# Kernel tuning notes

Measured on AMD Instinct MI355X. Metric: run time of the kernel, lower is better.

Reference implementation:

```python
import jax, jax.numpy as jnp
import numpy as np

B, N, C, H = 8, 1024, 768, 12
D = C // H
SCALE = D ** -0.5


def setup_inputs() -> dict:
    key = jax.random.key(0)
    k1, k2, k3 = jax.random.split(key, 3)
    x = jax.random.normal(k1, (B, N, C), dtype=jnp.float32)
    w_qkv = jax.random.normal(k2, (C, 3 * C), dtype=jnp.float32) * (C ** -0.5)
    w_proj = jax.random.normal(k3, (C, C), dtype=jnp.float32) * (C ** -0.5)
    b_proj = jnp.zeros((C,), dtype=jnp.float32)
    return {"x": x, "w_qkv": w_qkv, "w_proj": w_proj, "b_proj": b_proj}


def reference(x, w_qkv, w_proj, b_proj):
    Bx, Nx, Cx = x.shape
    # qkv projection (no bias), split into q,k,v with shape [B, H, N, D]
    qkv = (x @ w_qkv).reshape(Bx, Nx, 3, H, D).transpose(2, 0, 3, 1, 4)
    q, k, v = qkv[0], qkv[1], qkv[2]
    # full attention matrix [B, H, N, N] (matches torch module's explicit materialization)
    attn = jnp.einsum('bhqd,bhkd->bhqk', q, k) * SCALE
    attn = jax.nn.softmax(attn, axis=-1)
    out = jnp.einsum('bhqk,bhkd->bhqd', attn, v)
    out = out.transpose(0, 2, 1, 3).reshape(Bx, Nx, Cx)
    return out @ w_proj + b_proj
```

## Files before the change

kernel.cpp:

```cpp
#include <hip/hip_runtime.h>


typedef unsigned short u16;
typedef short s16x8 __attribute__((ext_vector_type(8)));
typedef float f32x4 __attribute__((ext_vector_type(4)));
typedef u16   u16x8 __attribute__((ext_vector_type(8)));
typedef u16   u16x4 __attribute__((ext_vector_type(4)));

__device__ __forceinline__ u16 f2bf(float f) {
    unsigned int u = __builtin_bit_cast(unsigned int, f);
    u += 0x7FFFu + ((u >> 16) & 1u);
    return (u16)(u >> 16);
}

__device__ __forceinline__ void gload16(const u16* g, u16* l) {
    __builtin_amdgcn_global_load_lds(
        (const __attribute__((address_space(1))) unsigned int*)g,
        (__attribute__((address_space(3))) unsigned int*)l, 16, 0, 0);
}

__global__ __launch_bounds__(256) void prep(
    const float* __restrict__ x, u16* __restrict__ xb,
    const float* __restrict__ wq, u16* __restrict__ wqT,
    const float* __restrict__ wp, u16* __restrict__ wpT) {
    __shared__ float ts[32][33];
    const int g = blockIdx.x, tid = threadIdx.x;
    if (g < 3072) {
        const size_t i = ((size_t)g * 256 + tid) * 8;
        float4 v0 = *(const float4*)(x + i);
        float4 v1 = *(const float4*)(x + i + 4);
        u16x8 p;
        p[0] = f2bf(v0.x); p[1] = f2bf(v0.y); p[2] = f2bf(v0.z); p[3] = f2bf(v0.w);
        p[4] = f2bf(v1.x); p[5] = f2bf(v1.y); p[6] = f2bf(v1.z); p[7] = f2bf(v1.w);
        *(u16x8*)(xb + i) = p;
        return;
    }
    const float* in; u16* out; int K, Nc, n0, k0;
    if (g < 4800) {
        int gg = g - 3072; in = wq; out = wqT; K = 768; Nc = 2304;
        n0 = (gg % 72) * 32; k0 = (gg / 72) * 32;
    } else {
        int gg = g - 4800; in = wp; out = wpT; K = 768; Nc = 768;
        n0 = (gg % 24) * 32; k0 = (gg / 24) * 32;
    }
    const int tx = tid & 31, ty = tid >> 5;
#pragma unroll
    for (int j = 0; j < 4; ++j) {
        int r = ty + j * 8;
        ts[r][tx] = in[(size_t)(k0 + r) * Nc + n0 + tx];
    }
    __syncthreads();
#pragma unroll
    for (int j = 0; j < 4; ++j) {
        int r = ty + j * 8;
        out[(size_t)(n0 + r) * K + k0 + tx] = f2bf(ts[tx][r]);
    }
}

template<bool SWAP>
__device__ __forceinline__ void gemm_loop_128(
    f32x4 (&acc)[4][4], const u16* __restrict__ A, const u16* __restrict__ B,
    u16* As, u16* Bs, int m0, int n0, int lane, int w) {
    const int m15 = lane & 15, quad = lane >> 4;
    const int wy = w >> 1, wx = w & 1;
    const int qsw8 = (quad ^ ((m15 >> 1) & 3)) * 8;
    const int srow16 = lane >> 2;
    const int scg = ((lane & 3) ^ ((lane >> 3) & 3)) * 8;
    const size_t gA = (size_t)(m0 + w * 32 + srow16) * 768 + scg;
    const size_t gB = (size_t)(n0 + w * 32 + srow16) * 768 + scg;

    auto stage = [&](int buf, int s) {
        const int k0 = (s < 24 ? s : 0) * 32;
        u16* da = As + buf * 4096 + (w * 32) * 32;
        u16* db = Bs + buf * 4096 + (w * 32) * 32;
        gload16(A + gA + k0,            da);
        gload16(A + gA + 16 * 768 + k0, da + 16 * 32);
        gload16(B + gB + k0,            db);
        gload16(B + gB + 16 * 768 + k0, db + 16 * 32);
    };

    stage(0, 0);
    stage(1, 1);
    const int arow = (wy * 64 + m15) * 32 + qsw8;
    const int brow = (wx * 64 + m15) * 32 + qsw8;

#pragma unroll 3
    for (int s = 0; s < 24; ++s) {
        const int cur = s % 3;
        stage((s + 2) % 3, s + 2);
        asm volatile("s_waitcnt vmcnt(8)" ::: "memory");
        __builtin_amdgcn_s_barrier();
        const u16* Ap = As + cur * 4096;
        const u16* Bp = Bs + cur * 4096;
        s16x8 av[4], bv[4];
#pragma unroll
        for (int ri = 0; ri < 4; ++ri)
            av[ri] = *(const s16x8*)(Ap + arow + ri * 512);
#pragma unroll
        for (int ci = 0; ci < 4; ++ci)
            bv[ci] = *(const s16x8*)(Bp + brow + ci * 512);
        __builtin_amdgcn_s_setprio(1);
#pragma unroll
        for (int ri = 0; ri < 4; ++ri)
#pragma unroll
            for (int ci = 0; ci < 4; ++ci) {
                if (SWAP)
                    acc[ri][ci] = __builtin_amdgcn_mfma_f32_16x16x32_bf16(bv[ci], av[ri], acc[ri][ci], 0, 0, 0);
                else
                    acc[ri][ci] = __builtin_amdgcn_mfma_f32_16x16x32_bf16(av[ri], bv[ci], acc[ri][ci], 0, 0, 0);
            }
        __builtin_amdgcn_s_setprio(0);
        __builtin_amdgcn_s_barrier();
    }
    asm volatile("s_waitcnt vmcnt(0)" ::: "memory");
}

__global__ __launch_bounds__(256, 3) void gemm_qkv(
    const u16* __restrict__ Aq, const u16* __restrict__ Bt,
    u16* __restrict__ qb, u16* __restrict__ kb, u16* __restrict__ vbT) {
    __shared__ __align__(16) u16 As[3 * 128 * 32];
    __shared__ __align__(16) u16 Bs[3 * 128 * 32];
    const int tid = threadIdx.x;
    const int lane = tid & 63, w = tid >> 6;
    const int m15 = lane & 15, quad = lane >> 4;
    const int wy = w >> 1, wx = w & 1;
    const int g = blockIdx.x;
    const int xcd = g & 7, s = g >> 3;
    const int yt = xcd * 8 + (s & 7), xt = s >> 3;
    const int m0 = yt * 128, n0 = xt * 128;
    const int which = xt / 6;

    f32x4 acc[4][4] = {};
    if (which < 2)
        gemm_loop_128<true >(acc, Aq, Bt, As, Bs, m0, n0, lane, w);
    else
        gemm_loop_128<false>(acc, Aq, Bt, As, Bs, m0, n0, lane, w);

    const int b   = m0 >> 10;
    const int r0  = (m0 & 1023) + wy * 64;
    const int n0p = n0 - which * 768;
    const int h   = (n0p >> 6) + wx;
    const size_t bhi = (size_t)(b * 12 + h);
    if (which == 2) {
#pragma unroll
        for (int ri = 0; ri < 4; ++ri)
#pragma unroll
            for (int ci = 0; ci < 4; ++ci) {
                u16x4 pk;
#pragma unroll
                for (int rg = 0; rg < 4; ++rg) pk[rg] = f2bf(acc[ri][ci][rg]);
                const int d   = ci * 16 + m15;
                const int tok = r0 + ri * 16 + (quad << 2);
                *(u16x4*)&vbT[(bhi * 64 + d) * 1024 + tok] = pk;
            }
    } else {
        u16* dst = which ? kb : qb;
#pragma unroll
        for (int ri = 0; ri < 4; ++ri)
#pragma unroll
            for (int ci = 0; ci < 4; ++ci) {
                u16x4 pk;
#pragma unroll
                for (int rg = 0; rg < 4; ++rg) pk[rg] = f2bf(acc[ri][ci][rg]);
                const int tok = r0 + ri * 16 + m15;
                const int d   = ci * 16 + (quad << 2);
                *(u16x4*)&dst[(bhi * 1024 + tok) * 64 + d] = pk;
            }
    }
}

__global__ __launch_bounds__(256, 3) void gemm_proj(
    const u16* __restrict__ A, const u16* __restrict__ Bt,
    const float* __restrict__ bias, float* __restrict__ out) {
    __shared__ __align__(16) u16 As[3 * 128 * 32];
    __shared__ __align__(16) u16 Bs[3 * 128 * 32];
    const int tid = threadIdx.x;
    const int lane = tid & 63, w = tid >> 6;
    const int m15 = lane & 15, quad = lane >> 4;
    const int wy = w >> 1, wx = w & 1;
    const int g = blockIdx.x;
    const int xcd = g & 7, s = g >> 3;
    const int yt = xcd * 8 + (s & 7), xt = s >> 3;
    const int m0 = yt * 128, n0 = xt * 128;

    f32x4 acc[4][4] = {};
    gemm_loop_128<false>(acc, A, Bt, As, Bs, m0, n0, lane, w);

#pragma unroll
    for (int ri = 0; ri < 4; ++ri) {
        int mb = m0 + wy * 64 + ri * 16 + (quad << 2);
#pragma unroll
        for (int ci = 0; ci < 4; ++ci) {
            int n = n0 + wx * 64 + ci * 16 + m15;
            float bv_ = bias[n];
#pragma unroll
            for (int rg = 0; rg < 4; ++rg)
                out[(size_t)(mb + rg) * 768 + n] = acc[ri][ci][rg] + bv_;
        }
    }
}

#define KS 72

__global__ __launch_bounds__(256) void attn_mfma(
    const u16* __restrict__ qb, const u16* __restrict__ kb,
    const u16* __restrict__ vbT, u16* __restrict__ aout) {
    __shared__ __align__(16) u16 Ks[64 * KS];
    __shared__ __align__(16) u16 Vs[64 * KS];
    __shared__ __align__(16) u16 Ps[8][16 * KS];
    const int tid = threadIdx.x, lane = tid & 63, w = tid >> 6;
    const int m15 = lane & 15, quad = lane >> 4;
    const int g = blockIdx.x;
    const int xcd = g & 7, s = g >> 3;
    const int bh = xcd * 12 + (s % 12);
    const int q0 = (s / 12) * 128;

    s16x8 aq[2][2];
#pragma unroll
    for (int qs = 0; qs < 2; ++qs) {
        const u16* qp = qb + ((size_t)bh * 1024 + q0 + w * 32 + qs * 16 + m15) * 64 + quad * 8;
        aq[qs][0] = *(const s16x8*)qp;
        aq[qs][1] = *(const s16x8*)(qp + 32);
    }

    s16x8 bones;
#pragma unroll
    for (int j = 0; j < 8; ++j) bones[j] = (m15 == 0) ? (short)0x3F80 : (short)0;

    f32x4 oacc[2][4] = {};
    f32x4 lacc[2] = {};

    const int srow = tid >> 2;
    const int soff = (tid & 3) * 16;
    const u16* kbase = kb + (size_t)bh * 1024 * 64;
    const u16* vbase = vbT + (size_t)bh * 64 * 1024;
    const float CE   = 0.125f * 1.44269504f;
    const float MOFF = 12.0f * 1.44269504f;

    for (int kt = 0; kt < 16; ++kt) {
        __syncthreads();
        const u16* kpp = kbase + ((size_t)kt * 64 + srow) * 64 + soff;
        const u16* vpp = vbase + (size_t)srow * 1024 + kt * 64 + soff;
        *(u16x8*)&Ks[srow * KS + soff]     = *(const u16x8*)kpp;
        *(u16x8*)&Ks[srow * KS + soff + 8] = *(const u16x8*)(kpp + 8);
        *(u16x8*)&Vs[srow * KS + soff]     = *(const u16x8*)vpp;
        *(u16x8*)&Vs[srow * KS + soff + 8] = *(const u16x8*)(vpp + 8);
        __syncthreads();

        f32x4 sacc[2][4] = {};
#pragma unroll
        for (int t = 0; t < 4; ++t)
#pragma unroll
            for (int ch = 0; ch < 2; ++ch) {
                s16x8 ak = *(const s16x8*)&Ks[(t * 16 + m15) * KS + quad * 8 + 32 * ch];
                sacc[0][t] = __builtin_amdgcn_mfma_f32_16x16x32_bf16(ak, aq[0][ch], sacc[0][t], 0, 0, 0);
                sacc[1][t] = __builtin_amdgcn_mfma_f32_16x16x32_bf16(ak, aq[1][ch], sacc[1][t], 0, 0, 0);
            }

#pragma unroll
        for (int qs = 0; qs < 2; ++qs)
#pragma unroll
            for (int t = 0; t < 4; ++t) {
                u16x4 pk;
#pragma unroll
                for (int reg = 0; reg < 4; ++reg) {
                    float pv = __builtin_amdgcn_exp2f(sacc[qs][t][reg] * CE - MOFF);
                    unsigned int u = __builtin_bit_cast(unsigned int, pv);
                    pk[reg] = (u16)(u >> 16);
                }
                *(u16x4*)&Ps[w * 2 + qs][m15 * KS + t * 16 + quad * 4] = pk;
            }

        s16x8 ap[2][2];
#pragma unroll
        for (int qs = 0; qs < 2; ++qs) {
            ap[qs][0] = *(const s16x8*)&Ps[w * 2 + qs][m15 * KS + quad * 8];
            ap[qs][1] = *(const s16x8*)&Ps[w * 2 + qs][m15 * KS + quad * 8 + 32];
#pragma unroll
            for (int ch = 0; ch < 2; ++ch)
                lacc[qs] = __builtin_amdgcn_mfma_f32_16x16x32_bf16(ap[qs][ch], bones, lacc[qs], 0, 0, 0);
        }
#pragma unroll
        for (int di = 0; di < 4; ++di)
#pragma unroll
            for (int ch = 0; ch < 2; ++ch) {
                s16x8 bv = *(const s16x8*)&Vs[(di * 16 + m15) * KS + quad * 8 + 32 * ch];
                oacc[0][di] = __builtin_amdgcn_mfma_f32_16x16x32_bf16(ap[0][ch], bv, oacc[0][di], 0, 0, 0);
                oacc[1][di] = __builtin_amdgcn_mfma_f32_16x16x32_bf16(ap[1][ch], bv, oacc[1][di], 0, 0, 0);
            }
    }

    const int b = bh / 12, h = bh - b * 12;
#pragma unroll
    for (int qs = 0; qs < 2; ++qs) {
        float linv[4];
#pragma unroll
        for (int reg = 0; reg < 4; ++reg)
            linv[reg] = 1.0f / __shfl(lacc[qs][reg], lane & 48);
#pragma unroll
        for (int di = 0; di < 4; ++di)
#pragma unroll
            for (int reg = 0; reg < 4; ++reg) {
                int q = q0 + w * 32 + qs * 16 + quad * 4 + reg;
                aout[((size_t)b * 1024 + q) * 768 + h * 64 + di * 16 + m15] =
                    f2bf(oacc[qs][di][reg] * linv[reg]);
            }
    }
}

extern "C" void kernel_launch(void* const* d_in, const int* in_sizes, int n_in,
                              void* d_out, int out_size, void* d_ws, size_t ws_size,
                              hipStream_t stream) {
    const float* x      = (const float*)d_in[0];
    const float* w_qkv  = (const float*)d_in[1];
    const float* w_proj = (const float*)d_in[2];
    const float* b_proj = (const float*)d_in[3];
    float* out = (float*)d_out;

    char* ws = (char*)d_ws;
    u16* wqkvT  = (u16*)ws;  ws += (size_t)2304 * 768 * 2;
    u16* wprojT = (u16*)ws;  ws += (size_t)768 * 768 * 2;
    u16* qb     = (u16*)ws;  ws += (size_t)96 * 1024 * 64 * 2;
    u16* kb     = (u16*)ws;  ws += (size_t)96 * 1024 * 64 * 2;
    u16* vbT    = (u16*)ws;  ws += (size_t)96 * 1024 * 64 * 2;
    u16* aout   = (u16*)ws;  ws += (size_t)8192 * 768 * 2;
    u16* xb     = aout;

    prep<<<dim3(5376), 256, 0, stream>>>(x, xb, w_qkv, wqkvT, w_proj, wprojT);
    gemm_qkv<<<dim3(1152), 256, 0, stream>>>(xb, wqkvT, qb, kb, vbT);
    attn_mfma<<<dim3(768), 256, 0, stream>>>(qb, kb, vbT, aout);
    gemm_proj<<<dim3(384), 256, 0, stream>>>(aout, wprojT, b_proj, out);
}
```

Baseline: 189.2 us.

## Double-buffer K/V tiles with async global-to-LDS loads and XOR swizzle

```diff
diff --git a/kernel.cpp b/kernel.cpp
--- a/kernel.cpp
+++ b/kernel.cpp
@@ -205,8 +205,8 @@
 __global__ __launch_bounds__(256) void attn_mfma(
     const u16* __restrict__ qb, const u16* __restrict__ kb,
     const u16* __restrict__ vbT, u16* __restrict__ aout) {
-    __shared__ __align__(16) u16 Ks[64 * KS];
-    __shared__ __align__(16) u16 Vs[64 * KS];
+    __shared__ __align__(16) u16 Ks[2][64 * 64];
+    __shared__ __align__(16) u16 Vs[2][64 * 64];
     __shared__ __align__(16) u16 Ps[8][16 * KS];
     const int tid = threadIdx.x, lane = tid & 63, w = tid >> 6;
     const int m15 = lane & 15, quad = lane >> 4;
@@ -230,29 +230,42 @@
     f32x4 oacc[2][4] = {};
     f32x4 lacc[2] = {};
 
-    const int srow = tid >> 2;
-    const int soff = (tid & 3) * 16;
     const u16* kbase = kb + (size_t)bh * 1024 * 64;
     const u16* vbase = vbT + (size_t)bh * 64 * 1024;
     const float CE   = 0.125f * 1.44269504f;
     const float MOFF = 12.0f * 1.44269504f;
 
+    const int r0w  = w * 16;
+    const int rloc = lane >> 3;
+    const int cswz = ((lane & 7) ^ rloc) * 8;
+    auto stageKV = [&](int buf, int kt) {
+        const int r1 = r0w + rloc, r2 = r0w + 8 + rloc;
+        gload16(kbase + ((size_t)kt * 64 + r1) * 64 + cswz, &Ks[buf][r0w * 64]);
+        gload16(kbase + ((size_t)kt * 64 + r2) * 64 + cswz, &Ks[buf][(r0w + 8) * 64]);
+        gload16(vbase + (size_t)r1 * 1024 + kt * 64 + cswz, &Vs[buf][r0w * 64]);
+        gload16(vbase + (size_t)r2 * 1024 + kt * 64 + cswz, &Vs[buf][(r0w + 8) * 64]);
+    };
+
+    stageKV(0, 0);
+
+    const int xr = m15 & 7;
+
     for (int kt = 0; kt < 16; ++kt) {
-        __syncthreads();
-        const u16* kpp = kbase + ((size_t)kt * 64 + srow) * 64 + soff;
-        const u16* vpp = vbase + (size_t)srow * 1024 + kt * 64 + soff;
-        *(u16x8*)&Ks[srow * KS + soff]     = *(const u16x8*)kpp;
-        *(u16x8*)&Ks[srow * KS + soff + 8] = *(const u16x8*)(kpp + 8);
-        *(u16x8*)&Vs[srow * KS + soff]     = *(const u16x8*)vpp;
-        *(u16x8*)&Vs[srow * KS + soff + 8] = *(const u16x8*)(vpp + 8);
-        __syncthreads();
+        const int cur = kt & 1;
+        stageKV(cur ^ 1, kt + 1 < 16 ? kt + 1 : 0);
+        asm volatile("s_waitcnt vmcnt(4)" ::: "memory");
+        __builtin_amdgcn_sched_barrier(0);
+        __builtin_amdgcn_s_barrier();
+        __builtin_amdgcn_sched_barrier(0);
+        const u16* Kp = Ks[cur];
+        const u16* Vp = Vs[cur];
 
         f32x4 sacc[2][4] = {};
 #pragma unroll
         for (int t = 0; t < 4; ++t)
 #pragma unroll
             for (int ch = 0; ch < 2; ++ch) {
-                s16x8 ak = *(const s16x8*)&Ks[(t * 16 + m15) * KS + quad * 8 + 32 * ch];
+                s16x8 ak = *(const s16x8*)&Kp[(t * 16 + m15) * 64 + ((quad + 4 * ch) ^ xr) * 8];
                 sacc[0][t] = __builtin_amdgcn_mfma_f32_16x16x32_bf16(ak, aq[0][ch], sacc[0][t], 0, 0, 0);
                 sacc[1][t] = __builtin_amdgcn_mfma_f32_16x16x32_bf16(ak, aq[1][ch], sacc[1][t], 0, 0, 0);
             }
@@ -284,11 +297,16 @@
         for (int di = 0; di < 4; ++di)
 #pragma unroll
             for (int ch = 0; ch < 2; ++ch) {
-                s16x8 bv = *(const s16x8*)&Vs[(di * 16 + m15) * KS + quad * 8 + 32 * ch];
+                s16x8 bv = *(const s16x8*)&Vp[(di * 16 + m15) * 64 + ((quad + 4 * ch) ^ xr) * 8];
                 oacc[0][di] = __builtin_amdgcn_mfma_f32_16x16x32_bf16(ap[0][ch], bv, oacc[0][di], 0, 0, 0);
                 oacc[1][di] = __builtin_amdgcn_mfma_f32_16x16x32_bf16(ap[1][ch], bv, oacc[1][di], 0, 0, 0);
             }
-    }
+
+        __builtin_amdgcn_sched_barrier(0);
+        __builtin_amdgcn_s_barrier();
+        __builtin_amdgcn_sched_barrier(0);
+    }
+    asm volatile("s_waitcnt vmcnt(0)" ::: "memory");
 
     const int b = bh / 12, h = bh - b * 12;
 #pragma unroll
```

New measurement: 194.3 us. +2.7%, slower.
